# Optimization experiments

Measured on AMD Instinct MI355X. Metric: run time of the kernel, lower is better.

Reference implementation:

```python
import jax, jax.numpy as jnp
import numpy as np

B, T, D, H, NH = 128, 64, 64, 128, 4


def setup_inputs() -> dict:
    key = jax.random.key(0)
    ks = jax.random.split(key, 32)
    s = 0.05
    inp = {
        "x": jax.random.normal(ks[0], (B, T, D), dtype=jnp.float32),
        "mask": jnp.ones((B, T), dtype=jnp.int32),
        # per-feature GRU params (input size 1, PyTorch gate order r,z,n)
        "Wih": jax.random.normal(ks[1], (D, 3 * H), dtype=jnp.float32) * s,
        "Whh": jax.random.normal(ks[2], (D, 3 * H, H), dtype=jnp.float32) * s,
        "bih": jax.random.normal(ks[3], (D, 3 * H), dtype=jnp.float32) * s,
        "bhh": jax.random.normal(ks[4], (D, 3 * H), dtype=jnp.float32) * s,
        # MHA projections (stored [in,out]; y = x @ W + b)
        "Wq": jax.random.normal(ks[5], (H, H), dtype=jnp.float32) * s,
        "bq": jnp.zeros((H,), dtype=jnp.float32),
        "Wk": jax.random.normal(ks[6], (H, H), dtype=jnp.float32) * s,
        "bk": jnp.zeros((H,), dtype=jnp.float32),
        "Wv": jax.random.normal(ks[7], (H, H), dtype=jnp.float32) * s,
        "bv": jnp.zeros((H,), dtype=jnp.float32),
        "Wo": jax.random.normal(ks[8], (H, H), dtype=jnp.float32) * s,
        "bo": jnp.zeros((H,), dtype=jnp.float32),
        # FFN
        "W1": jax.random.normal(ks[9], (H, 2 * H), dtype=jnp.float32) * s,
        "b1": jnp.zeros((2 * H,), dtype=jnp.float32),
        "W2": jax.random.normal(ks[10], (2 * H, H), dtype=jnp.float32) * s,
        "b2": jnp.zeros((H,), dtype=jnp.float32),
        # LayerNorms
        "g1": jnp.ones((H,), dtype=jnp.float32),
        "be1": jnp.zeros((H,), dtype=jnp.float32),
        "g2": jnp.ones((H,), dtype=jnp.float32),
        "be2": jnp.zeros((H,), dtype=jnp.float32),
        # FinalAttentionQKV
        "Fq": jax.random.normal(ks[11], (H, H), dtype=jnp.float32) * s,
        "fbq": jnp.zeros((H,), dtype=jnp.float32),
        "Fk": jax.random.normal(ks[12], (H, H), dtype=jnp.float32) * s,
        "fbk": jnp.zeros((H,), dtype=jnp.float32),
        "Fv": jax.random.normal(ks[13], (H, H), dtype=jnp.float32) * s,
        "fbv": jnp.zeros((H,), dtype=jnp.float32),
        "Fout": jax.random.normal(ks[14], (H,), dtype=jnp.float32) * s,
        "fbout": jnp.zeros((), dtype=jnp.float32),
    }
    return inp


def _layernorm(x, g, b, eps=1e-5):
    m = jnp.mean(x, axis=-1, keepdims=True)
    v = jnp.mean((x - m) ** 2, axis=-1, keepdims=True)
    return (x - m) * jax.lax.rsqrt(v + eps) * g + b


def _forward(x, mask, Wih, Whh, bih, bhh, Wq, bq, Wk, bk, Wv, bv, Wo, bo,
             W1, b1, W2, b2, g1, be1, g2, be2,
             Fq, fbq, Fk, fbk, Fv, fbv, Fout, fbout):
    Bc, Tc, Dc = x.shape
    Hc = Whh.shape[-1]

    # --- D independent GRUs, fused: batch axes (B, D), scalar input per step ---
    def step(h, xt):  # h: [B,D,H], xt: [B,D]
        gx = xt[..., None] * Wih + bih                     # [B,D,3H]
        gh = jnp.einsum('bdh,dkh->bdk', h, Whh) + bhh      # [B,D,3H]
        r = jax.nn.sigmoid(gx[..., :Hc] + gh[..., :Hc])
        z = jax.nn.sigmoid(gx[..., Hc:2 * Hc] + gh[..., Hc:2 * Hc])
        n = jnp.tanh(gx[..., 2 * Hc:] + r * gh[..., 2 * Hc:])
        hn = (1.0 - z) * n + z * h
        return hn, hn

    xs = jnp.transpose(x, (1, 0, 2))                        # [T,B,D]
    h0 = jnp.zeros((Bc, Dc, Hc), dtype=x.dtype)
    _, ys = jax.lax.scan(step, h0, xs)                      # [T,B,D,H]

    # last_by_lengths: gather hidden state at index lengths-1 per batch element
    lengths = jnp.sum(mask, axis=1)                         # [B]
    idx = jnp.clip(lengths - 1, 0, Tc - 1)
    emb = ys[idx, jnp.arange(Bc)]                           # [B,D,H] (D tokens)

    # --- MHA (self-attention over D feature tokens); dropout = identity (eval) ---
    dk = Hc // NH
    def split_heads(t):
        return jnp.transpose(t.reshape(Bc, Dc, NH, dk), (0, 2, 1, 3))  # [B,NH,D,dk]
    q = split_heads(emb @ Wq + bq)
    k = split_heads(emb @ Wk + bk)
    v = split_heads(emb @ Wv + bv)
    scores = jnp.einsum('bhnd,bhmd->bhnm', q, k) / jnp.sqrt(jnp.float32(dk))
    attn = jax.nn.softmax(scores, axis=-1)
    o = jnp.einsum('bhnm,bhmd->bhnd', attn, v)
    o = jnp.transpose(o, (0, 2, 1, 3)).reshape(Bc, Dc, Hc)
    mha_out = o @ Wo + bo

    h1 = _layernorm(emb + mha_out, g1, be1)
    ffn = jax.nn.relu(h1 @ W1 + b1) @ W2 + b2
    h2 = _layernorm(h1 + ffn, g2, be2)

    # --- FinalAttentionQKV ---
    fq = (h2[:, -1, :] @ Fq + fbq)[:, None, :]              # [B,1,H]
    fk = h2 @ Fk + fbk                                      # [B,D,H]
    fv = h2 @ Fv + fbv                                      # [B,D,H]
    e = jnp.tanh(fq + fk) @ Fout + fbout                    # [B,D]
    a = jax.nn.softmax(e, axis=-1)
    return jnp.einsum('bn,bnh->bh', a, fv)                  # [B,H]


def reference(x, mask, Wih, Whh, bih, bhh, Wq, bq, Wk, bk, Wv, bv, Wo, bo,
              W1, b1, W2, b2, g1, be1, g2, be2,
              Fq, fbq, Fk, fbk, Fv, fbv, Fout, fbout):
    return _forward(x, mask, Wih, Whh, bih, bhh, Wq, bq, Wk, bk, Wv, bv, Wo, bo,
                    W1, b1, W2, b2, g1, be1, g2, be2,
                    Fq, fbq, Fk, fbk, Fv, fbv, Fout, fbout)
```

## Files before the change

kernel.cpp:

```cpp
#include <hip/hip_runtime.h>
#include <math.h>

#define BB 128
#define TT 64
#define DD 64
#define HH 128
#define NHH 4
#define K3H 384

typedef __attribute__((ext_vector_type(8))) short short8_t;
typedef __attribute__((ext_vector_type(4))) float float4_t;

#define LOG2E 1.4426950408889634f

__device__ __forceinline__ unsigned short f2bf(float f) {
    unsigned int u = __float_as_uint(f);
    u += 0x7fffu + ((u >> 16) & 1u);
    return (unsigned short)(u >> 16);
}

__device__ __forceinline__ unsigned pack_bf2(float lo, float hi) {
    return (unsigned)f2bf(lo) | ((unsigned)f2bf(hi) << 16);
}

__device__ __forceinline__ float bf2f(unsigned short s) {
    return __uint_as_float((unsigned)s << 16);
}

__global__ __launch_bounds__(512, 4) void gru_mfma_kernel(
    const float* __restrict__ x, const int* __restrict__ mask,
    const float* __restrict__ Wih, const float* __restrict__ Whh,
    const float* __restrict__ bih, const float* __restrict__ bhh,
    float* __restrict__ emb)
{
    const int d  = blockIdx.x;
    const int b0 = blockIdx.y * 16;
    const int tid = threadIdx.x;
    const int w = tid >> 6;
    const int l = tid & 63;
    const int m = l & 15;
    const int q = l >> 4;

    __shared__ __align__(16) unsigned short hbuf[2][16][136];
    __shared__ float xs_t[TT][16];
    __shared__ int tstar_s[16];

    for (int idx = tid; idx < 16 * TT; idx += 512) {
        int t = idx >> 4, row = idx & 15;
        xs_t[t][row] = x[((size_t)(b0 + row) * TT + t) * DD + d];
    }
    if (tid < 16) {
        int b = b0 + tid, len = 0;
        for (int t = 0; t < TT; ++t) len += mask[b * TT + t];
        int ts = len - 1;
        if (ts < 0) ts = 0;
        if (ts > TT - 1) ts = TT - 1;
        tstar_s[tid] = ts;
    }
    for (int idx = tid; idx < 16 * 136; idx += 512)
        ((unsigned short*)hbuf)[idx] = 0;

    short8_t Wf[3][4];
#pragma unroll
    for (int g = 0; g < 3; ++g) {
        float sc = (g == 2) ? (2.f * LOG2E) : (-LOG2E);
        int kcol = g * HH + 16 * w + m;
        const float* wrow = Whh + ((size_t)d * K3H + kcol) * HH;
#pragma unroll
        for (int kc = 0; kc < 4; ++kc) {
            int j0 = kc * 32 + q * 8;
            float4 w0 = *(const float4*)(wrow + j0);
            float4 w1 = *(const float4*)(wrow + j0 + 4);
            short8_t f;
            f[0] = (short)f2bf(w0.x * sc); f[1] = (short)f2bf(w0.y * sc);
            f[2] = (short)f2bf(w0.z * sc); f[3] = (short)f2bf(w0.w * sc);
            f[4] = (short)f2bf(w1.x * sc); f[5] = (short)f2bf(w1.y * sc);
            f[6] = (short)f2bf(w1.z * sc); f[7] = (short)f2bf(w1.w * sc);
            Wf[g][kc] = f;
        }
    }

    const int hcol0 = 16 * w + q * 4;
    float4 wr4 = *(const float4*)&Wih[d * K3H + hcol0];
    float4 wz4 = *(const float4*)&Wih[d * K3H + HH + hcol0];
    float4 wn4 = *(const float4*)&Wih[d * K3H + 2 * HH + hcol0];
    float4 br4 = *(const float4*)&bih[d * K3H + hcol0];
    float4 bz4 = *(const float4*)&bih[d * K3H + HH + hcol0];
    float4 bni4 = *(const float4*)&bih[d * K3H + 2 * HH + hcol0];
    float4 bhr4 = *(const float4*)&bhh[d * K3H + hcol0];
    float4 bhz4 = *(const float4*)&bhh[d * K3H + HH + hcol0];
    float4 bnh4 = *(const float4*)&bhh[d * K3H + 2 * HH + hcol0];
    float brs[4], bzs[4], bnis[4], bnhs[4], wrs[4], wzs[4], wns[4];
#pragma unroll
    for (int r = 0; r < 4; ++r) {
        wrs[r] = -LOG2E * ((const float*)&wr4)[r];
        wzs[r] = -LOG2E * ((const float*)&wz4)[r];
        wns[r] = 2.f * LOG2E * ((const float*)&wn4)[r];
        brs[r] = -LOG2E * (((const float*)&br4)[r] + ((const float*)&bhr4)[r]);
        bzs[r] = -LOG2E * (((const float*)&bz4)[r] + ((const float*)&bhz4)[r]);
        bnis[r] = 2.f * LOG2E * ((const float*)&bni4)[r];
        bnhs[r] = 2.f * LOG2E * ((const float*)&bnh4)[r];
    }

    float hprev[4];
#pragma unroll
    for (int i = 0; i < 4; ++i) hprev[i] = 0.f;

    __syncthreads();
    const int tstar_m = tstar_s[m];
    float* embp = emb + (((size_t)(b0 + m)) * DD + d) * HH + hcol0;

    for (int t = 0; t < TT; ++t) {
        const unsigned short* hb = &hbuf[t & 1][0][0];
        unsigned short* hbn = &hbuf[(t & 1) ^ 1][0][0];

        short8_t hf[4];
#pragma unroll
        for (int kc = 0; kc < 4; ++kc)
            hf[kc] = *(const short8_t*)(hb + m * 136 + kc * 32 + q * 8);
        float xv = xs_t[t][m];

        float4_t ar = {0.f,0.f,0.f,0.f}, az = {0.f,0.f,0.f,0.f}, an = {0.f,0.f,0.f,0.f};
#pragma unroll
        for (int kc = 0; kc < 4; ++kc) {
            ar = __builtin_amdgcn_mfma_f32_16x16x32_bf16(Wf[0][kc], hf[kc], ar, 0, 0, 0);
            az = __builtin_amdgcn_mfma_f32_16x16x32_bf16(Wf[1][kc], hf[kc], az, 0, 0, 0);
            an = __builtin_amdgcn_mfma_f32_16x16x32_bf16(Wf[2][kc], hf[kc], an, 0, 0, 0);
        }

        float hn4[4];
#pragma unroll
        for (int reg = 0; reg < 4; ++reg) {
            float grs = ar[reg] + fmaf(xv, wrs[reg], brs[reg]);
            float gzs = az[reg] + fmaf(xv, wzs[reg], bzs[reg]);
            float rg = __builtin_amdgcn_rcpf(1.f + __builtin_amdgcn_exp2f(grs));
            float zg = __builtin_amdgcn_rcpf(1.f + __builtin_amdgcn_exp2f(gzs));
            float gns = fmaf(rg, an[reg] + bnhs[reg], fmaf(xv, wns[reg], bnis[reg]));
            float tn = fmaf(-2.f, __builtin_amdgcn_rcpf(__builtin_amdgcn_exp2f(gns) + 1.f), 1.f);
            float hn = fmaf(zg, hprev[reg] - tn, tn);
            hprev[reg] = hn;
            hn4[reg] = hn;
        }
        uint2 uu;
        uu.x = pack_bf2(hn4[0], hn4[1]);
        uu.y = pack_bf2(hn4[2], hn4[3]);
        *(uint2*)(hbn + m * 136 + hcol0) = uu;
        if (t == tstar_m) {
            float4 hv; hv.x = hn4[0]; hv.y = hn4[1]; hv.z = hn4[2]; hv.w = hn4[3];
            *(float4*)embp = hv;
        }
        __syncthreads();
    }
}


__device__ __forceinline__ void stage_w(unsigned short (*Wt)[136],
                                        const float* __restrict__ Wp,
                                        int Nst, int n0, float scale, int tid)
{
    for (int it = tid; it < 4096; it += 512) {
        int n = it & 127, k4 = (it >> 7) << 2;
        const float* p = Wp + (size_t)k4 * Nst + n0 + n;
        float w0 = p[0], w1 = p[Nst], w2 = p[2 * Nst], w3 = p[3 * Nst];
        uint2 pk;
        pk.x = pack_bf2(w0 * scale, w1 * scale);
        pk.y = pack_bf2(w2 * scale, w3 * scale);
        *(uint2*)&Wt[n][k4] = pk;
    }
}

__device__ __forceinline__ void load_afrag(const unsigned short (*S)[136],
                                           short8_t Af[4][4], int m16, int q)
{
#pragma unroll
    for (int mt = 0; mt < 4; ++mt)
#pragma unroll
        for (int kc = 0; kc < 4; ++kc)
            Af[mt][kc] = *(const short8_t*)&S[mt * 16 + m16][kc * 32 + q * 8];
}

__device__ __forceinline__ void mm_acc(const unsigned short (*Wt)[136],
                                       short8_t Af[4][4], float4_t acc[4],
                                       int w, int m16, int q)
{
    short8_t Bf[4];
#pragma unroll
    for (int kc = 0; kc < 4; ++kc)
        Bf[kc] = *(const short8_t*)&Wt[w * 16 + m16][kc * 32 + q * 8];
#pragma unroll
    for (int mt = 0; mt < 4; ++mt) {
        float4_t a = acc[mt];
#pragma unroll
        for (int kc = 0; kc < 4; ++kc)
            a = __builtin_amdgcn_mfma_f32_16x16x32_bf16(Af[mt][kc], Bf[kc], a, 0, 0, 0);
        acc[mt] = a;
    }
}

__device__ __forceinline__ void zero4(float4_t acc[4]) {
#pragma unroll
    for (int mt = 0; mt < 4; ++mt) acc[mt] = (float4_t){0.f, 0.f, 0.f, 0.f};
}

__device__ __forceinline__ void store_bf(unsigned short (*Dst)[136], float4_t acc[4],
                                         const float* __restrict__ bias, int n0,
                                         float bscale, int relu,
                                         int w, int m16, int q)
{
    float bv = bias[n0 + w * 16 + m16] * bscale;
#pragma unroll
    for (int mt = 0; mt < 4; ++mt)
#pragma unroll
        for (int reg = 0; reg < 4; ++reg) {
            float v = acc[mt][reg] + bv;
            if (relu) v = fmaxf(v, 0.f);
            Dst[mt * 16 + q * 4 + reg][w * 16 + m16] = f2bf(v);
        }
}

__global__ __launch_bounds__(512) void tail_kernel(
    const float* __restrict__ emb,
    const float* __restrict__ Wq, const float* __restrict__ bq,
    const float* __restrict__ Wk, const float* __restrict__ bk,
    const float* __restrict__ Wv, const float* __restrict__ bv,
    const float* __restrict__ Wo, const float* __restrict__ bo,
    const float* __restrict__ W1, const float* __restrict__ b1,
    const float* __restrict__ W2, const float* __restrict__ b2,
    const float* __restrict__ g1, const float* __restrict__ be1,
    const float* __restrict__ g2, const float* __restrict__ be2,
    const float* __restrict__ Fq, const float* __restrict__ fbq,
    const float* __restrict__ Fk, const float* __restrict__ fbk,
    const float* __restrict__ Fv, const float* __restrict__ fbv,
    const float* __restrict__ Fout, const float* __restrict__ fbout,
    float* __restrict__ h1g, float* __restrict__ out)
{
    const int b = blockIdx.x;
    const int tid = threadIdx.x;
    const int w = tid >> 6, l = tid & 63, m16 = l & 15, q = l >> 4;
    const int col = w * 16 + m16;

    __shared__ __align__(16) unsigned short E[64][136];
    __shared__ __align__(16) unsigned short Qs[64][136];
    __shared__ __align__(16) unsigned short Ks[64][136];
    __shared__ __align__(16) unsigned short Vs[64][136];
    __shared__ __align__(16) unsigned short Wt[128][136];
    __shared__ float sc[64][66];
    __shared__ float lnp[64][8], lnp2[64][8];
    __shared__ float inv_s[64], mean_s[64], rs_s[64];
    __shared__ float fq_s[128], fo_s[128], e_s[64], red_s[256];

    const float* embB = emb + (size_t)b * 64 * 128;
    float* h1gB = h1g + (size_t)b * 64 * 128;
    const float SS = 0.17677669529663687f;

    for (int it = tid; it < 2048; it += 512) {
        int r = it >> 5, c4 = (it & 31) << 2;
        float4 a = *(const float4*)&embB[r * 128 + c4];
        uint2 p; p.x = pack_bf2(a.x, a.y); p.y = pack_bf2(a.z, a.w);
        *(uint2*)&E[r][c4] = p;
    }
    stage_w(Wt, Wq, 128, 0, SS, tid);
    __syncthreads();

    short8_t AfE[4][4];
    float4_t acc[4];
    load_afrag(E, AfE, m16, q);

    zero4(acc); mm_acc(Wt, AfE, acc, w, m16, q);
    store_bf(Qs, acc, bq, 0, SS, 0, w, m16, q);
    __syncthreads();
    stage_w(Wt, Wk, 128, 0, 1.f, tid);
    __syncthreads();
    zero4(acc); mm_acc(Wt, AfE, acc, w, m16, q);
    store_bf(Ks, acc, bk, 0, 1.f, 0, w, m16, q);
    __syncthreads();
    stage_w(Wt, Wv, 128, 0, 1.f, tid);
    __syncthreads();
    zero4(acc); mm_acc(Wt, AfE, acc, w, m16, q);
    store_bf(Vs, acc, bv, 0, 1.f, 0, w, m16, q);
    __syncthreads();

    for (int hd = 0; hd < 4; ++hd) {
        {
            int mt = w >> 1;
            short8_t Aq = *(const short8_t*)&Qs[mt * 16 + m16][hd * 32 + q * 8];
#pragma unroll
            for (int nn = 0; nn < 2; ++nn) {
                int nt = (w & 1) * 2 + nn;
                short8_t Bk = *(const short8_t*)&Ks[nt * 16 + m16][hd * 32 + q * 8];
                float4_t a = {0.f, 0.f, 0.f, 0.f};
                a = __builtin_amdgcn_mfma_f32_16x16x32_bf16(Aq, Bk, a, 0, 0, 0);
#pragma unroll
                for (int reg = 0; reg < 4; ++reg)
                    sc[mt * 16 + q * 4 + reg][nt * 16 + m16] = a[reg];
            }
        }
        __syncthreads();
        {
            int row = tid >> 3, c8 = tid & 7;
            float vals[8]; float mx = -1e30f;
#pragma unroll
            for (int c = 0; c < 8; ++c) { vals[c] = sc[row][c8 + 8 * c]; mx = fmaxf(mx, vals[c]); }
            mx = fmaxf(mx, __shfl_xor(mx, 1));
            mx = fmaxf(mx, __shfl_xor(mx, 2));
            mx = fmaxf(mx, __shfl_xor(mx, 4));
            float sum = 0.f;
#pragma unroll
            for (int c = 0; c < 8; ++c) {
                float p = __expf(vals[c] - mx);
                sc[row][c8 + 8 * c] = p;
                sum += p;
            }
            sum += __shfl_xor(sum, 1); sum += __shfl_xor(sum, 2); sum += __shfl_xor(sum, 4);
            if (c8 == 0) inv_s[row] = __builtin_amdgcn_rcpf(sum);
        }
        __syncthreads();
        {
            float o0 = 0.f, o1 = 0.f, o2 = 0.f, o3 = 0.f;
            for (int j = 0; j < 64; ++j) {
                float p = sc[l][j];
                uint2 vv = *(const uint2*)&Vs[j][hd * 32 + w * 4];
                o0 = fmaf(p, __uint_as_float(vv.x << 16), o0);
                o1 = fmaf(p, __uint_as_float(vv.x & 0xffff0000u), o1);
                o2 = fmaf(p, __uint_as_float(vv.y << 16), o2);
                o3 = fmaf(p, __uint_as_float(vv.y & 0xffff0000u), o3);
            }
            float iv = inv_s[l];
            uint2 pk; pk.x = pack_bf2(o0 * iv, o1 * iv); pk.y = pack_bf2(o2 * iv, o3 * iv);
            *(uint2*)&E[l][hd * 32 + w * 4] = pk;
        }
        __syncthreads();
    }

    stage_w(Wt, Wo, 128, 0, 1.f, tid);
    __syncthreads();
    short8_t AfX[4][4];
    load_afrag(E, AfX, m16, q);
    zero4(acc); mm_acc(Wt, AfX, acc, w, m16, q);
    float vals[4][4];
    {
        float bv = bo[col];
#pragma unroll
        for (int mt = 0; mt < 4; ++mt)
#pragma unroll
            for (int reg = 0; reg < 4; ++reg) {
                int row = mt * 16 + q * 4 + reg;
                vals[mt][reg] = acc[mt][reg] + bv + embB[row * 128 + col];
            }
    }
#pragma unroll
    for (int mt = 0; mt < 4; ++mt)
#pragma unroll
        for (int reg = 0; reg < 4; ++reg) {
            float s = vals[mt][reg], s2 = s * s;
            s += __shfl_xor(s, 1); s += __shfl_xor(s, 2); s += __shfl_xor(s, 4); s += __shfl_xor(s, 8);
            s2 += __shfl_xor(s2, 1); s2 += __shfl_xor(s2, 2); s2 += __shfl_xor(s2, 4); s2 += __shfl_xor(s2, 8);
            if (m16 == 0) { int row = mt * 16 + q * 4 + reg; lnp[row][w] = s; lnp2[row][w] = s2; }
        }
    __syncthreads();
    if (tid < 64) {
        float s = 0.f, s2 = 0.f;
#pragma unroll
        for (int k = 0; k < 8; ++k) { s += lnp[tid][k]; s2 += lnp2[tid][k]; }
        float mn = s * (1.f / 128.f);
        float var = s2 * (1.f / 128.f) - mn * mn;
        mean_s[tid] = mn;
        rs_s[tid] = rsqrtf(var + 1e-5f);
    }
    __syncthreads();
    {
        float gv = g1[col], bev = be1[col];
#pragma unroll
        for (int mt = 0; mt < 4; ++mt)
#pragma unroll
            for (int reg = 0; reg < 4; ++reg) {
                int row = mt * 16 + q * 4 + reg;
                float hv = (vals[mt][reg] - mean_s[row]) * rs_s[row] * gv + bev;
                E[row][col] = f2bf(hv);
                h1gB[(size_t)row * 128 + col] = hv;
            }
    }

    stage_w(Wt, W1, 256, 0, 1.f, tid);
    __syncthreads();
    load_afrag(E, AfX, m16, q);
    zero4(acc); mm_acc(Wt, AfX, acc, w, m16, q);
    store_bf(Qs, acc, b1, 0, 1.f, 1, w, m16, q);
    __syncthreads();
    stage_w(Wt, W1, 256, 128, 1.f, tid);
    __syncthreads();
    zero4(acc); mm_acc(Wt, AfX, acc, w, m16, q);
    store_bf(Ks, acc, b1, 128, 1.f, 1, w, m16, q);
    __syncthreads();

    stage_w(Wt, W2, 128, 0, 1.f, tid);
    __syncthreads();
    short8_t AfY[4][4];
    load_afrag(Qs, AfY, m16, q);
    zero4(acc); mm_acc(Wt, AfY, acc, w, m16, q);
    __syncthreads();
    stage_w(Wt, W2 + (size_t)128 * 128, 128, 0, 1.f, tid);
    __syncthreads();
    load_afrag(Ks, AfY, m16, q);
    mm_acc(Wt, AfY, acc, w, m16, q);
    {
        float bv = b2[col];
#pragma unroll
        for (int mt = 0; mt < 4; ++mt)
#pragma unroll
            for (int reg = 0; reg < 4; ++reg) {
                int row = mt * 16 + q * 4 + reg;
                vals[mt][reg] = acc[mt][reg] + bv + h1gB[(size_t)row * 128 + col];
            }
    }
#pragma unroll
    for (int mt = 0; mt < 4; ++mt)
#pragma unroll
        for (int reg = 0; reg < 4; ++reg) {
            float s = vals[mt][reg], s2 = s * s;
            s += __shfl_xor(s, 1); s += __shfl_xor(s, 2); s += __shfl_xor(s, 4); s += __shfl_xor(s, 8);
            s2 += __shfl_xor(s2, 1); s2 += __shfl_xor(s2, 2); s2 += __shfl_xor(s2, 4); s2 += __shfl_xor(s2, 8);
            if (m16 == 0) { int row = mt * 16 + q * 4 + reg; lnp[row][w] = s; lnp2[row][w] = s2; }
        }
    __syncthreads();
    if (tid < 64) {
        float s = 0.f, s2 = 0.f;
#pragma unroll
        for (int k = 0; k < 8; ++k) { s += lnp[tid][k]; s2 += lnp2[tid][k]; }
        float mn = s * (1.f / 128.f);
        float var = s2 * (1.f / 128.f) - mn * mn;
        mean_s[tid] = mn;
        rs_s[tid] = rsqrtf(var + 1e-5f);
    }
    __syncthreads();
    {
        float gv = g2[col], bev = be2[col];
#pragma unroll
        for (int mt = 0; mt < 4; ++mt)
#pragma unroll
            for (int reg = 0; reg < 4; ++reg) {
                int row = mt * 16 + q * 4 + reg;
                float hv = (vals[mt][reg] - mean_s[row]) * rs_s[row] * gv + bev;
                E[row][col] = f2bf(hv);
            }
    }

    stage_w(Wt, Fk, 128, 0, 1.f, tid);
    __syncthreads();
    load_afrag(E, AfX, m16, q);
    zero4(acc); mm_acc(Wt, AfX, acc, w, m16, q);
    store_bf(Qs, acc, fbk, 0, 1.f, 0, w, m16, q);
    __syncthreads();
    stage_w(Wt, Fv, 128, 0, 1.f, tid);
    if (tid < 128) fo_s[tid] = Fout[tid];
    __syncthreads();
    zero4(acc); mm_acc(Wt, AfX, acc, w, m16, q);
    store_bf(Ks, acc, fbv, 0, 1.f, 0, w, m16, q);
    __syncthreads();

    if (tid < 128) {
        float a = fbq[tid];
        for (int mm2 = 0; mm2 < 128; ++mm2)
            a = fmaf(bf2f(E[63][mm2]), Fq[mm2 * 128 + tid], a);
        fq_s[tid] = a;
    }
    __syncthreads();
    {
        int dd = tid >> 3, c8 = tid & 7;
        float p = 0.f;
#pragma unroll
        for (int c = 0; c < 16; ++c) {
            int cc = c8 * 16 + c;
            float t = fq_s[cc] + bf2f(Qs[dd][cc]);
            float tn = 1.f - 2.f * __builtin_amdgcn_rcpf(
                __builtin_amdgcn_exp2f(2.f * LOG2E * t) + 1.f);
            p = fmaf(tn, fo_s[cc], p);
        }
        p += __shfl_xor(p, 1); p += __shfl_xor(p, 2); p += __shfl_xor(p, 4);
        if (c8 == 0) e_s[dd] = p + fbout[0];
    }
    __syncthreads();
    if (tid < 64) {
        float e = e_s[tid], mx = e;
        for (int o = 32; o; o >>= 1) mx = fmaxf(mx, __shfl_xor(mx, o));
        float pe = __expf(e - mx);
        float s = pe;
        for (int o = 32; o; o >>= 1) s += __shfl_xor(s, o);
        e_s[tid] = pe / s;
    }
    __syncthreads();
    if (tid < 256) {
        int c2 = tid & 127, rg2 = tid >> 7;
        float a = 0.f;
        for (int d2 = rg2 * 32; d2 < rg2 * 32 + 32; ++d2)
            a = fmaf(e_s[d2], bf2f(Ks[d2][c2]), a);
        red_s[tid] = a;
    }
    __syncthreads();
    if (tid < 128)
        out[(size_t)b * 128 + tid] = red_s[tid] + red_s[tid + 128];
}

extern "C" void kernel_launch(void* const* d_in, const int* in_sizes, int n_in,
                              void* d_out, int out_size, void* d_ws, size_t ws_size,
                              hipStream_t stream)
{
    const float* x    = (const float*)d_in[0];
    const int*   mask = (const int*)d_in[1];
    const float* Wih  = (const float*)d_in[2];
    const float* Whh  = (const float*)d_in[3];
    const float* bih  = (const float*)d_in[4];
    const float* bhh  = (const float*)d_in[5];
    const float* Wq = (const float*)d_in[6];   const float* bq = (const float*)d_in[7];
    const float* Wk = (const float*)d_in[8];   const float* bk = (const float*)d_in[9];
    const float* Wv = (const float*)d_in[10];  const float* bv = (const float*)d_in[11];
    const float* Wo = (const float*)d_in[12];  const float* bo = (const float*)d_in[13];
    const float* W1 = (const float*)d_in[14];  const float* b1 = (const float*)d_in[15];
    const float* W2 = (const float*)d_in[16];  const float* b2 = (const float*)d_in[17];
    const float* g1 = (const float*)d_in[18];  const float* be1 = (const float*)d_in[19];
    const float* g2 = (const float*)d_in[20];  const float* be2 = (const float*)d_in[21];
    const float* Fq = (const float*)d_in[22];  const float* fbq = (const float*)d_in[23];
    const float* Fk = (const float*)d_in[24];  const float* fbk = (const float*)d_in[25];
    const float* Fv = (const float*)d_in[26];  const float* fbv = (const float*)d_in[27];
    const float* Fout = (const float*)d_in[28]; const float* fbout = (const float*)d_in[29];
    float* out = (float*)d_out;
    float* ws  = (float*)d_ws;

    float* emb = ws;
    float* h1g = ws + 1048576;

    gru_mfma_kernel<<<dim3(DD, BB / 16), 512, 0, stream>>>(x, mask, Wih, Whh, bih, bhh, emb);
    tail_kernel<<<BB, 512, 0, stream>>>(
        emb, Wq, bq, Wk, bk, Wv, bv, Wo, bo, W1, b1, W2, b2,
        g1, be1, g2, be2, Fq, fbq, Fk, fbk, Fv, fbv, Fout, fbout,
        h1g, out);
}
```

Before: 269.3 us.

## Hold tail-kernel weight fragments in registers and run all heads' attention on MFMA at once

In the tail kernel, each wave now loads its B-operand weight fragments straight from global memory into registers instead of staging every 128x128 weight into shared memory behind barriers. Weights for later stages are fetched early so their latency can overlap earlier compute. All four heads' scores and softmax are computed together, and P·V now uses MFMA on a transposed V tile instead of a scalar FMA loop. The residual h1 stays in registers rather than going through a global scratch buffer. This trades several syncs and shared-memory traffic for more register pressure and uncoalesced strided global weight reads, all inside a tail kernel that is likely small next to the GRU kernel.

```diff
diff --git a/kernel.cpp b/kernel.cpp
--- a/kernel.cpp
+++ b/kernel.cpp
@@ -154,18 +154,18 @@
 }
 
 
-__device__ __forceinline__ void stage_w(unsigned short (*Wt)[136],
-                                        const float* __restrict__ Wp,
-                                        int Nst, int n0, float scale, int tid)
-{
-    for (int it = tid; it < 4096; it += 512) {
-        int n = it & 127, k4 = (it >> 7) << 2;
-        const float* p = Wp + (size_t)k4 * Nst + n0 + n;
-        float w0 = p[0], w1 = p[Nst], w2 = p[2 * Nst], w3 = p[3 * Nst];
-        uint2 pk;
-        pk.x = pack_bf2(w0 * scale, w1 * scale);
-        pk.y = pack_bf2(w2 * scale, w3 * scale);
-        *(uint2*)&Wt[n][k4] = pk;
+__device__ __forceinline__ void load_wfrag(const float* __restrict__ Wp, int N,
+                                           int col, float scale, int q,
+                                           short8_t fr[4])
+{
+#pragma unroll
+    for (int kc = 0; kc < 4; ++kc) {
+        const float* p = Wp + (size_t)(kc * 32 + q * 8) * N + col;
+        short8_t f;
+#pragma unroll
+        for (int j = 0; j < 8; ++j)
+            f[j] = (short)f2bf(p[(size_t)j * N] * scale);
+        fr[kc] = f;
     }
 }
 
@@ -179,14 +179,9 @@
             Af[mt][kc] = *(const short8_t*)&S[mt * 16 + m16][kc * 32 + q * 8];
 }
 
-__device__ __forceinline__ void mm_acc(const unsigned short (*Wt)[136],
-                                       short8_t Af[4][4], float4_t acc[4],
-                                       int w, int m16, int q)
-{
-    short8_t Bf[4];
-#pragma unroll
-    for (int kc = 0; kc < 4; ++kc)
-        Bf[kc] = *(const short8_t*)&Wt[w * 16 + m16][kc * 32 + q * 8];
+__device__ __forceinline__ void mm_regw(short8_t Af[4][4], short8_t Bf[4],
+                                        float4_t acc[4])
+{
 #pragma unroll
     for (int mt = 0; mt < 4; ++mt) {
         float4_t a = acc[mt];
@@ -202,19 +197,16 @@
     for (int mt = 0; mt < 4; ++mt) acc[mt] = (float4_t){0.f, 0.f, 0.f, 0.f};
 }
 
-__device__ __forceinline__ void store_bf(unsigned short (*Dst)[136], float4_t acc[4],
-                                         const float* __restrict__ bias, int n0,
-                                         float bscale, int relu,
-                                         int w, int m16, int q)
-{
-    float bv = bias[n0 + w * 16 + m16] * bscale;
+__device__ __forceinline__ void store_rows(unsigned short (*Dst)[136], float4_t acc[4],
+                                           float bv, int relu, int col, int q)
+{
 #pragma unroll
     for (int mt = 0; mt < 4; ++mt)
 #pragma unroll
         for (int reg = 0; reg < 4; ++reg) {
             float v = acc[mt][reg] + bv;
             if (relu) v = fmaxf(v, 0.f);
-            Dst[mt * 16 + q * 4 + reg][w * 16 + m16] = f2bf(v);
+            Dst[mt * 16 + q * 4 + reg][col] = f2bf(v);
         }
 }
 
@@ -232,7 +224,7 @@
     const float* __restrict__ Fk, const float* __restrict__ fbk,
     const float* __restrict__ Fv, const float* __restrict__ fbv,
     const float* __restrict__ Fout, const float* __restrict__ fbout,
-    float* __restrict__ h1g, float* __restrict__ out)
+    float* __restrict__ out)
 {
     const int b = blockIdx.x;
     const int tid = threadIdx.x;
@@ -242,16 +234,20 @@
     __shared__ __align__(16) unsigned short E[64][136];
     __shared__ __align__(16) unsigned short Qs[64][136];
     __shared__ __align__(16) unsigned short Ks[64][136];
-    __shared__ __align__(16) unsigned short Vs[64][136];
-    __shared__ __align__(16) unsigned short Wt[128][136];
-    __shared__ float sc[64][66];
+    __shared__ __align__(16) unsigned short Vt[128][72];
+    __shared__ float sc4[4][64][66];
     __shared__ float lnp[64][8], lnp2[64][8];
-    __shared__ float inv_s[64], mean_s[64], rs_s[64];
+    __shared__ float mean_s[64], rs_s[64];
     __shared__ float fq_s[128], fo_s[128], e_s[64], red_s[256];
 
     const float* embB = emb + (size_t)b * 64 * 128;
-    float* h1gB = h1g + (size_t)b * 64 * 128;
     const float SS = 0.17677669529663687f;
+
+    short8_t WqF[4], WkF[4], WvF[4];
+    load_wfrag(Wq, 128, col, SS, q, WqF);
+    load_wfrag(Wk, 128, col, 1.f, q, WkF);
+    load_wfrag(Wv, 128, col, 1.f, q, WvF);
+    float bqv = bq[col] * SS, bkv = bk[col], bvv = bv[col];
 
     for (int it = tid; it < 2048; it += 512) {
         int r = it >> 5, c4 = (it & 31) << 2;
@@ -259,100 +255,114 @@
         uint2 p; p.x = pack_bf2(a.x, a.y); p.y = pack_bf2(a.z, a.w);
         *(uint2*)&E[r][c4] = p;
     }
-    stage_w(Wt, Wq, 128, 0, SS, tid);
-    __syncthreads();
-
-    short8_t AfE[4][4];
+    __syncthreads();
+
+    short8_t Af[4][4];
     float4_t acc[4];
-    load_afrag(E, AfE, m16, q);
-
-    zero4(acc); mm_acc(Wt, AfE, acc, w, m16, q);
-    store_bf(Qs, acc, bq, 0, SS, 0, w, m16, q);
-    __syncthreads();
-    stage_w(Wt, Wk, 128, 0, 1.f, tid);
-    __syncthreads();
-    zero4(acc); mm_acc(Wt, AfE, acc, w, m16, q);
-    store_bf(Ks, acc, bk, 0, 1.f, 0, w, m16, q);
-    __syncthreads();
-    stage_w(Wt, Wv, 128, 0, 1.f, tid);
-    __syncthreads();
-    zero4(acc); mm_acc(Wt, AfE, acc, w, m16, q);
-    store_bf(Vs, acc, bv, 0, 1.f, 0, w, m16, q);
-    __syncthreads();
-
-    for (int hd = 0; hd < 4; ++hd) {
-        {
-            int mt = w >> 1;
+    load_afrag(E, Af, m16, q);
+
+    zero4(acc); mm_regw(Af, WqF, acc); store_rows(Qs, acc, bqv, 0, col, q);
+    zero4(acc); mm_regw(Af, WkF, acc); store_rows(Ks, acc, bkv, 0, col, q);
+    zero4(acc); mm_regw(Af, WvF, acc);
+#pragma unroll
+    for (int mt = 0; mt < 4; ++mt) {
+        uint2 pk;
+        pk.x = pack_bf2(acc[mt][0] + bvv, acc[mt][1] + bvv);
+        pk.y = pack_bf2(acc[mt][2] + bvv, acc[mt][3] + bvv);
+        *(uint2*)&Vt[col][mt * 16 + q * 4] = pk;
+    }
+    __syncthreads();
+
+    short8_t WoF[4], W1aF[4], W1bF[4];
+    load_wfrag(Wo, 128, col, 1.f, q, WoF);
+    load_wfrag(W1, 256, col, 1.f, q, W1aF);
+    load_wfrag(W1, 256, 128 + col, 1.f, q, W1bF);
+    float bov = bo[col], b1a = b1[col], b1b = b1[128 + col];
+    float g1v = g1[col], be1v = be1[col];
+
+    {
+        int hd = w >> 1, ntb = (w & 1) * 2;
+#pragma unroll
+        for (int mt = 0; mt < 4; ++mt) {
             short8_t Aq = *(const short8_t*)&Qs[mt * 16 + m16][hd * 32 + q * 8];
 #pragma unroll
             for (int nn = 0; nn < 2; ++nn) {
-                int nt = (w & 1) * 2 + nn;
+                int nt = ntb + nn;
                 short8_t Bk = *(const short8_t*)&Ks[nt * 16 + m16][hd * 32 + q * 8];
                 float4_t a = {0.f, 0.f, 0.f, 0.f};
                 a = __builtin_amdgcn_mfma_f32_16x16x32_bf16(Aq, Bk, a, 0, 0, 0);
 #pragma unroll
                 for (int reg = 0; reg < 4; ++reg)
-                    sc[mt * 16 + q * 4 + reg][nt * 16 + m16] = a[reg];
+                    sc4[hd][mt * 16 + q * 4 + reg][nt * 16 + m16] = a[reg];
             }
         }
-        __syncthreads();
-        {
-            int row = tid >> 3, c8 = tid & 7;
-            float vals[8]; float mx = -1e30f;
-#pragma unroll
-            for (int c = 0; c < 8; ++c) { vals[c] = sc[row][c8 + 8 * c]; mx = fmaxf(mx, vals[c]); }
-            mx = fmaxf(mx, __shfl_xor(mx, 1));
-            mx = fmaxf(mx, __shfl_xor(mx, 2));
-            mx = fmaxf(mx, __shfl_xor(mx, 4));
-            float sum = 0.f;
-#pragma unroll
-            for (int c = 0; c < 8; ++c) {
-                float p = __expf(vals[c] - mx);
-                sc[row][c8 + 8 * c] = p;
-                sum += p;
-            }
-            sum += __shfl_xor(sum, 1); sum += __shfl_xor(sum, 2); sum += __shfl_xor(sum, 4);
-            if (c8 == 0) inv_s[row] = __builtin_amdgcn_rcpf(sum);
-        }
-        __syncthreads();
-        {
-            float o0 = 0.f, o1 = 0.f, o2 = 0.f, o3 = 0.f;
-            for (int j = 0; j < 64; ++j) {
-                float p = sc[l][j];
-                uint2 vv = *(const uint2*)&Vs[j][hd * 32 + w * 4];
-                o0 = fmaf(p, __uint_as_float(vv.x << 16), o0);
-                o1 = fmaf(p, __uint_as_float(vv.x & 0xffff0000u), o1);
-                o2 = fmaf(p, __uint_as_float(vv.y << 16), o2);
-                o3 = fmaf(p, __uint_as_float(vv.y & 0xffff0000u), o3);
-            }
-            float iv = inv_s[l];
-            uint2 pk; pk.x = pack_bf2(o0 * iv, o1 * iv); pk.y = pack_bf2(o2 * iv, o3 * iv);
-            *(uint2*)&E[l][hd * 32 + w * 4] = pk;
-        }
-        __syncthreads();
-    }
-
-    stage_w(Wt, Wo, 128, 0, 1.f, tid);
-    __syncthreads();
-    short8_t AfX[4][4];
-    load_afrag(E, AfX, m16, q);
-    zero4(acc); mm_acc(Wt, AfX, acc, w, m16, q);
-    float vals[4][4];
+    }
+    __syncthreads();
+
     {
-        float bv = bo[col];
-#pragma unroll
-        for (int mt = 0; mt < 4; ++mt)
-#pragma unroll
-            for (int reg = 0; reg < 4; ++reg) {
-                int row = mt * 16 + q * 4 + reg;
-                vals[mt][reg] = acc[mt][reg] + bv + embB[row * 128 + col];
-            }
-    }
-#pragma unroll
-    for (int mt = 0; mt < 4; ++mt)
-#pragma unroll
-        for (int reg = 0; reg < 4; ++reg) {
-            float s = vals[mt][reg], s2 = s * s;
+        int pr = tid >> 1, hd2 = pr >> 6, row = pr & 63, half = (tid & 1) * 32;
+        float v[32]; float mx = -1e30f;
+#pragma unroll
+        for (int c = 0; c < 32; ++c) { v[c] = sc4[hd2][row][half + c]; mx = fmaxf(mx, v[c]); }
+        mx = fmaxf(mx, __shfl_xor(mx, 1));
+        float sum = 0.f;
+#pragma unroll
+        for (int c = 0; c < 32; ++c) { v[c] = __expf(v[c] - mx); sum += v[c]; }
+        sum += __shfl_xor(sum, 1);
+        float inv = __builtin_amdgcn_rcpf(sum);
+        unsigned short (*Pd)[136] = (hd2 < 2) ? Qs : Ks;
+        int cb = (hd2 & 1) * 64 + half;
+#pragma unroll
+        for (int c = 0; c < 16; ++c)
+            *(unsigned*)&Pd[row][cb + 2 * c] = pack_bf2(v[2 * c] * inv, v[2 * c + 1] * inv);
+    }
+    __syncthreads();
+
+    {
+        int hd = w >> 1, nt = w & 1;
+        const unsigned short (*P)[136] = (hd < 2) ? (const unsigned short (*)[136])Qs
+                                                  : (const unsigned short (*)[136])Ks;
+        int pb = (hd & 1) * 64;
+        int vrow = hd * 32 + nt * 16 + m16;
+        short8_t B0f = *(const short8_t*)&Vt[vrow][q * 8];
+        short8_t B1f = *(const short8_t*)&Vt[vrow][32 + q * 8];
+#pragma unroll
+        for (int mt = 0; mt < 4; ++mt) {
+            short8_t A0 = *(const short8_t*)&P[mt * 16 + m16][pb + q * 8];
+            short8_t A1 = *(const short8_t*)&P[mt * 16 + m16][pb + 32 + q * 8];
+            float4_t a = {0.f, 0.f, 0.f, 0.f};
+            a = __builtin_amdgcn_mfma_f32_16x16x32_bf16(A0, B0f, a, 0, 0, 0);
+            a = __builtin_amdgcn_mfma_f32_16x16x32_bf16(A1, B1f, a, 0, 0, 0);
+#pragma unroll
+            for (int reg = 0; reg < 4; ++reg)
+                E[mt * 16 + q * 4 + reg][vrow] = f2bf(a[reg]);
+        }
+    }
+    __syncthreads();
+
+    short8_t W2aF[4], W2bF[4], FkF[4], FvF[4];
+    load_wfrag(W2, 128, col, 1.f, q, W2aF);
+    load_wfrag(W2 + (size_t)128 * 128, 128, col, 1.f, q, W2bF);
+    load_wfrag(Fk, 128, col, 1.f, q, FkF);
+    load_wfrag(Fv, 128, col, 1.f, q, FvF);
+    float b2v = b2[col], fbkv = fbk[col], fbvv = fbv[col];
+    float g2v = g2[col], be2v = be2[col];
+
+    load_afrag(E, Af, m16, q);
+    zero4(acc); mm_regw(Af, WoF, acc);
+    float h1v[4][4];
+#pragma unroll
+    for (int mt = 0; mt < 4; ++mt)
+#pragma unroll
+        for (int reg = 0; reg < 4; ++reg) {
+            int row = mt * 16 + q * 4 + reg;
+            h1v[mt][reg] = acc[mt][reg] + bov + embB[(size_t)row * 128 + col];
+        }
+#pragma unroll
+    for (int mt = 0; mt < 4; ++mt)
+#pragma unroll
+        for (int reg = 0; reg < 4; ++reg) {
+            float s = h1v[mt][reg], s2 = s * s;
             s += __shfl_xor(s, 1); s += __shfl_xor(s, 2); s += __shfl_xor(s, 4); s += __shfl_xor(s, 8);
             s2 += __shfl_xor(s2, 1); s2 += __shfl_xor(s2, 2); s2 += __shfl_xor(s2, 4); s2 += __shfl_xor(s2, 8);
             if (m16 == 0) { int row = mt * 16 + q * 4 + reg; lnp[row][w] = s; lnp2[row][w] = s2; }
@@ -363,61 +373,42 @@
 #pragma unroll
         for (int k = 0; k < 8; ++k) { s += lnp[tid][k]; s2 += lnp2[tid][k]; }
         float mn = s * (1.f / 128.f);
-        float var = s2 * (1.f / 128.f) - mn * mn;
         mean_s[tid] = mn;
-        rs_s[tid] = rsqrtf(var + 1e-5f);
-    }
-    __syncthreads();
+        rs_s[tid] = rsqrtf(s2 * (1.f / 128.f) - mn * mn + 1e-5f);
+    }
+    __syncthreads();
+#pragma unroll
+    for (int mt = 0; mt < 4; ++mt)
+#pragma unroll
+        for (int reg = 0; reg < 4; ++reg) {
+            int row = mt * 16 + q * 4 + reg;
+            float hv = (h1v[mt][reg] - mean_s[row]) * rs_s[row] * g1v + be1v;
+            h1v[mt][reg] = hv;
+            E[row][col] = f2bf(hv);
+        }
+    __syncthreads();
+
+    load_afrag(E, Af, m16, q);
+    zero4(acc); mm_regw(Af, W1aF, acc); store_rows(Qs, acc, b1a, 1, col, q);
+    zero4(acc); mm_regw(Af, W1bF, acc); store_rows(Ks, acc, b1b, 1, col, q);
+    __syncthreads();
+
     {
-        float gv = g1[col], bev = be1[col];
-#pragma unroll
-        for (int mt = 0; mt < 4; ++mt)
-#pragma unroll
-            for (int reg = 0; reg < 4; ++reg) {
-                int row = mt * 16 + q * 4 + reg;
-                float hv = (vals[mt][reg] - mean_s[row]) * rs_s[row] * gv + bev;
-                E[row][col] = f2bf(hv);
-                h1gB[(size_t)row * 128 + col] = hv;
-            }
-    }
-
-    stage_w(Wt, W1, 256, 0, 1.f, tid);
-    __syncthreads();
-    load_afrag(E, AfX, m16, q);
-    zero4(acc); mm_acc(Wt, AfX, acc, w, m16, q);
-    store_bf(Qs, acc, b1, 0, 1.f, 1, w, m16, q);
-    __syncthreads();
-    stage_w(Wt, W1, 256, 128, 1.f, tid);
-    __syncthreads();
-    zero4(acc); mm_acc(Wt, AfX, acc, w, m16, q);
-    store_bf(Ks, acc, b1, 128, 1.f, 1, w, m16, q);
-    __syncthreads();
-
-    stage_w(Wt, W2, 128, 0, 1.f, tid);
-    __syncthreads();
-    short8_t AfY[4][4];
-    load_afrag(Qs, AfY, m16, q);
-    zero4(acc); mm_acc(Wt, AfY, acc, w, m16, q);
-    __syncthreads();
-    stage_w(Wt, W2 + (size_t)128 * 128, 128, 0, 1.f, tid);
-    __syncthreads();
-    load_afrag(Ks, AfY, m16, q);
-    mm_acc(Wt, AfY, acc, w, m16, q);
-    {
-        float bv = b2[col];
-#pragma unroll
-        for (int mt = 0; mt < 4; ++mt)
-#pragma unroll
-            for (int reg = 0; reg < 4; ++reg) {
-                int row = mt * 16 + q * 4 + reg;
-                vals[mt][reg] = acc[mt][reg] + bv + h1gB[(size_t)row * 128 + col];
-            }
-    }
-#pragma unroll
-    for (int mt = 0; mt < 4; ++mt)
-#pragma unroll
-        for (int reg = 0; reg < 4; ++reg) {
-            float s = vals[mt][reg], s2 = s * s;
+        short8_t AfQ[4][4], AfK[4][4];
+        load_afrag(Qs, AfQ, m16, q);
+        load_afrag(Ks, AfK, m16, q);
+        zero4(acc); mm_regw(AfQ, W2aF, acc); mm_regw(AfK, W2bF, acc);
+    }
+#pragma unroll
+    for (int mt = 0; mt < 4; ++mt)
+#pragma unroll
+        for (int reg = 0; reg < 4; ++reg)
+            h1v[mt][reg] = acc[mt][reg] + b2v + h1v[mt][reg];
+#pragma unroll
+    for (int mt = 0; mt < 4; ++mt)
+#pragma unroll
+        for (int reg = 0; reg < 4; ++reg) {
+            float s = h1v[mt][reg], s2 = s * s;
             s += __shfl_xor(s, 1); s += __shfl_xor(s, 2); s += __shfl_xor(s, 4); s += __shfl_xor(s, 8);
             s2 += __shfl_xor(s2, 1); s2 += __shfl_xor(s2, 2); s2 += __shfl_xor(s2, 4); s2 += __shfl_xor(s2, 8);
             if (m16 == 0) { int row = mt * 16 + q * 4 + reg; lnp[row][w] = s; lnp2[row][w] = s2; }
@@ -428,43 +419,32 @@
 #pragma unroll
         for (int k = 0; k < 8; ++k) { s += lnp[tid][k]; s2 += lnp2[tid][k]; }
         float mn = s * (1.f / 128.f);
-        float var = s2 * (1.f / 128.f) - mn * mn;
         mean_s[tid] = mn;
-        rs_s[tid] = rsqrtf(var + 1e-5f);
-    }
-    __syncthreads();
-    {
-        float gv = g2[col], bev = be2[col];
-#pragma unroll
-        for (int mt = 0; mt < 4; ++mt)
-#pragma unroll
-            for (int reg = 0; reg < 4; ++reg) {
-                int row = mt * 16 + q * 4 + reg;
-                float hv = (vals[mt][reg] - mean_s[row]) * rs_s[row] * gv + bev;
-                E[row][col] = f2bf(hv);
-            }
-    }
-
-    stage_w(Wt, Fk, 128, 0, 1.f, tid);
-    __syncthreads();
-    load_afrag(E, AfX, m16, q);
-    zero4(acc); mm_acc(Wt, AfX, acc, w, m16, q);
-    store_bf(Qs, acc, fbk, 0, 1.f, 0, w, m16, q);
-    __syncthreads();
-    stage_w(Wt, Fv, 128, 0, 1.f, tid);
-    if (tid < 128) fo_s[tid] = Fout[tid];
-    __syncthreads();
-    zero4(acc); mm_acc(Wt, AfX, acc, w, m16, q);
-    store_bf(Ks, acc, fbv, 0, 1.f, 0, w, m16, q);
-    __syncthreads();
-
+        rs_s[tid] = rsqrtf(s2 * (1.f / 128.f) - mn * mn + 1e-5f);
+    }
+    __syncthreads();
+#pragma unroll
+    for (int mt = 0; mt < 4; ++mt)
+#pragma unroll
+        for (int reg = 0; reg < 4; ++reg) {
+            int row = mt * 16 + q * 4 + reg;
+            float hv = (h1v[mt][reg] - mean_s[row]) * rs_s[row] * g2v + be2v;
+            E[row][col] = f2bf(hv);
+        }
+    __syncthreads();
+
+    load_afrag(E, Af, m16, q);
+    zero4(acc); mm_regw(Af, FkF, acc); store_rows(Qs, acc, fbkv, 0, col, q);
+    zero4(acc); mm_regw(Af, FvF, acc); store_rows(Ks, acc, fbvv, 0, col, q);
     if (tid < 128) {
+        fo_s[tid] = Fout[tid];
         float a = fbq[tid];
         for (int mm2 = 0; mm2 < 128; ++mm2)
             a = fmaf(bf2f(E[63][mm2]), Fq[mm2 * 128 + tid], a);
         fq_s[tid] = a;
     }
     __syncthreads();
+
     {
         int dd = tid >> 3, c8 = tid & 7;
         float p = 0.f;
@@ -527,11 +507,9 @@
     float* ws  = (float*)d_ws;
 
     float* emb = ws;
-    float* h1g = ws + 1048576;
 
     gru_mfma_kernel<<<dim3(DD, BB / 16), 512, 0, stream>>>(x, mask, Wih, Whh, bih, bhh, emb);
     tail_kernel<<<BB, 512, 0, stream>>>(
         emb, Wq, bq, Wk, bk, Wv, bv, Wo, bo, W1, b1, W2, b2,
-        g1, be1, g2, be2, Fq, fbq, Fk, fbk, Fv, fbv, Fout, fbout,
-        h1g, out);
-}
+        g1, be1, g2, be2, Fq, fbq, Fk, fbk, Fv, fbv, Fout, fbout, out);
+}
```

After: 250.9 us. 6.8% less time.
